# Kernel optimization log

Hardware: AMD Instinct MI355X
Metric: run time of the kernel (lower is better)

The kernel has to match this reference:

```python
import jax, jax.numpy as jnp
import numpy as np

N = 50000
DIM_IN = 256
HID = 64
OUT = 32
E1 = 800000
E2 = 1600000
BN_EPS = 1e-5


def _make_edges(rng, n, e):
    row = rng.integers(0, n, size=e).astype(np.int32)
    col = rng.integers(0, n, size=e).astype(np.int32)
    # gcn_norm without self loops: val = d^{-1/2}[row] * d^{-1/2}[col]
    deg = np.bincount(row, minlength=n) + 0.0
    deg_c = np.bincount(col, minlength=n) + 0.0
    dr = 1.0 / np.sqrt(np.maximum(deg, 1.0))
    dc = 1.0 / np.sqrt(np.maximum(deg_c, 1.0))
    val = (dr[row] * dc[col]).astype(np.float32)
    return row, col, val


def setup_inputs() -> dict:
    key = jax.random.key(0)
    ks = jax.random.split(key, 4)
    rng = np.random.default_rng(0)
    e1_row, e1_col, e1_val = _make_edges(rng, N, E1)
    e2_row, e2_col, e2_val = _make_edges(rng, N, E2)
    return {
        "x": jax.random.normal(ks[0], (N, DIM_IN), dtype=jnp.float32),
        "e1_row": jnp.asarray(e1_row), "e1_col": jnp.asarray(e1_col), "e1_val": jnp.asarray(e1_val),
        "e2_row": jnp.asarray(e2_row), "e2_col": jnp.asarray(e2_col), "e2_val": jnp.asarray(e2_val),
        "W_embed": jax.random.normal(ks[1], (DIM_IN, HID), dtype=jnp.float32) * (1.0 / np.sqrt(DIM_IN)),
        "b_embed": jnp.zeros((HID,), dtype=jnp.float32),
        "bn0_gamma": jnp.ones((2 * HID,), dtype=jnp.float32),
        "bn0_beta": jnp.zeros((2 * HID,), dtype=jnp.float32),
        "bn1_gamma": jnp.ones((4 * HID,), dtype=jnp.float32),
        "bn1_beta": jnp.zeros((4 * HID,), dtype=jnp.float32),
        "W_head": jax.random.normal(ks[2], (15 * HID, OUT), dtype=jnp.float32) * (1.0 / np.sqrt(15 * HID)),
        "b_head": jnp.zeros((OUT,), dtype=jnp.float32),
    }


def _spmm(row, col, val, x, n):
    # out[row] += val * x[col]  (sparse [n,n] @ dense [n,d])
    return jax.ops.segment_sum(val[:, None] * x[col], row, num_segments=n)


def _bn(v, gamma, beta):
    # BatchNorm1d training-mode math: per-feature mean / biased var over nodes
    m = jnp.mean(v, axis=0)
    var = jnp.mean(jnp.square(v - m), axis=0)
    return gamma * (v - m) * jax.lax.rsqrt(var + BN_EPS) + beta


def reference(x, e1_row, e1_col, e1_val, e2_row, e2_col, e2_val,
              W_embed, b_embed, bn0_gamma, bn0_beta, bn1_gamma, bn1_beta,
              W_head, b_head):
    n = x.shape[0]

    def conv(h):
        h1 = _spmm(e1_row, e1_col, e1_val, h, n)
        h2 = _spmm(e2_row, e2_col, e2_val, h, n)
        return jnp.concatenate([h1, h2], axis=1)

    h = jax.nn.relu(x @ W_embed + b_embed)          # [n, HID]
    xs = [h]
    c0 = _bn(conv(h), bn0_gamma, bn0_beta)           # [n, 2*HID]
    xs.append(c0)
    c1 = _bn(conv(c0), bn1_gamma, bn1_beta)          # [n, 4*HID]
    xs.append(c1)
    c2 = conv(c1)                                    # [n, 8*HID]
    xs.append(c2)
    j = jnp.concatenate(xs, axis=1)                  # [n, 15*HID]
    return j @ W_head + b_head                       # [n, OUT]
```

## Files before the change

kernel.cpp:

```cpp
#include <hip/hip_runtime.h>


#define NN  50000
#define E1N 800000
#define E2N 1600000
#define LD  960
#define NT  3125
#define NBKT 391
#define CHUNK 8192
#define G1B 98
#define G2B 196
#define NCG 7

typedef short bf16x8 __attribute__((ext_vector_type(8)));
typedef float f32x4  __attribute__((ext_vector_type(4)));
typedef float f32x2  __attribute__((ext_vector_type(2)));

__device__ __forceinline__ float bfl(unsigned int w) { return __uint_as_float(w << 16); }
__device__ __forceinline__ float bfh(unsigned int w) { return __uint_as_float(w & 0xFFFF0000u); }
__device__ __forceinline__ float bf2f(unsigned short u) { return __uint_as_float(((unsigned int)u) << 16); }
__device__ __forceinline__ unsigned short f2bf(float f) {
    unsigned int u = __float_as_uint(f);
    u += 0x7FFFu + ((u >> 16) & 1u);
    return (unsigned short)(u >> 16);
}
__device__ __forceinline__ unsigned int pack2(float a, float b) {
    return (unsigned int)f2bf(a) | ((unsigned int)f2bf(b) << 16);
}
__device__ __forceinline__ unsigned int packfp8(float a, float b, float c, float d) {
    int w = __builtin_amdgcn_cvt_pk_fp8_f32(a, b, 0, false);
    w     = __builtin_amdgcn_cvt_pk_fp8_f32(c, d, w, true);
    return (unsigned int)w;
}
__device__ __forceinline__ f32x2 pkfma(f32x2 a, f32x2 b, f32x2 c) {
#if __has_builtin(__builtin_elementwise_fma)
    return __builtin_elementwise_fma(a, b, c);
#else
    return (f32x2){fmaf(a[0], b[0], c[0]), fmaf(a[1], b[1], c[1])};
#endif
}
__device__ __forceinline__ f32x2 bf2(unsigned int w) {
    return (f32x2){bfl(w), bfh(w)};
}


__global__ __launch_bounds__(256) void zero_kernel(float* c, int nc) {
    int i = blockIdx.x * 256 + threadIdx.x;
    if (i < nc) c[i] = 0.f;
}

__global__ __launch_bounds__(256) void bucket_count_kernel(const int* __restrict__ r1,
                                                           const int* __restrict__ r2,
                                                           int* __restrict__ bc1, int* __restrict__ bc2) {
    __shared__ int cnt[NBKT];
    for (int t = threadIdx.x; t < NBKT; t += 256) cnt[t] = 0;
    __syncthreads();
    int blk = blockIdx.x;
    const int* r; int base, lim; int* bc;
    if (blk < G1B) { r = r1; base = blk * CHUNK; lim = min(base + CHUNK, E1N); bc = bc1 + blk * NBKT; }
    else { int b2 = blk - G1B; r = r2; base = b2 * CHUNK; lim = min(base + CHUNK, E2N); bc = bc2 + b2 * NBKT; }
    for (int i = base + threadIdx.x; i < lim; i += 256)
        atomicAdd(&cnt[r[i] >> 7], 1);
    __syncthreads();
    for (int t = threadIdx.x; t < NBKT; t += 256) bc[t] = cnt[t];
}

__global__ __launch_bounds__(512) void bucket_scan_kernel(int* __restrict__ bc1, int* __restrict__ bc2) {
    __shared__ int s[512];
    int t = threadIdx.x;
    int tot1 = 0, tot2 = 0;
    if (t < NBKT) {
        for (int b = 0; b < G1B; b++) tot1 += bc1[b * NBKT + t];
        for (int b = 0; b < G2B; b++) tot2 += bc2[b * NBKT + t];
    }
    s[t] = (t < NBKT) ? tot1 : 0;
    __syncthreads();
    for (int off = 1; off < 512; off <<= 1) {
        int v = (t >= off) ? s[t - off] : 0;
        __syncthreads(); s[t] += v; __syncthreads();
    }
    int base1 = ((t < NBKT) ? s[t] : 0) - tot1;
    __syncthreads();
    s[t] = (t < NBKT) ? tot2 : 0;
    __syncthreads();
    for (int off = 1; off < 512; off <<= 1) {
        int v = (t >= off) ? s[t - off] : 0;
        __syncthreads(); s[t] += v; __syncthreads();
    }
    int base2 = ((t < NBKT) ? s[t] : 0) - tot2;
    if (t < NBKT) {
        int run = base1;
        for (int b = 0; b < G1B; b++) { int v = bc1[b * NBKT + t]; bc1[b * NBKT + t] = run; run += v; }
        run = base2;
        for (int b = 0; b < G2B; b++) { int v = bc2[b * NBKT + t]; bc2[b * NBKT + t] = run; run += v; }
    }
}

__global__ __launch_bounds__(256) void bucket_place_kernel(
        const int* __restrict__ r1, const int* __restrict__ c1, const float* __restrict__ v1,
        const int* __restrict__ r2, const int* __restrict__ c2, const float* __restrict__ v2,
        const int* __restrict__ bc1, const int* __restrict__ bc2,
        uint2* __restrict__ T1, uint2* __restrict__ T2) {
    __shared__ int pos[NBKT];
    int blk = blockIdx.x;
    const int *r, *c; const float* v; int base, lim; const int* bc; uint2* T;
    if (blk < G1B) { r = r1; c = c1; v = v1; base = blk * CHUNK; lim = min(base + CHUNK, E1N);
                     bc = bc1 + blk * NBKT; T = T1; }
    else { int b2 = blk - G1B; r = r2; c = c2; v = v2; base = b2 * CHUNK; lim = min(base + CHUNK, E2N);
           bc = bc2 + b2 * NBKT; T = T2; }
    for (int t = threadIdx.x; t < NBKT; t += 256) pos[t] = bc[t];
    __syncthreads();
    for (int i = base + threadIdx.x; i < lim; i += 256) {
        int row = r[i];
        int p = atomicAdd(&pos[row >> 7], 1);
        T[p] = make_uint2(((unsigned)c[i] << 16) | (unsigned)row, __float_as_uint(v[i]));
    }
}

__global__ __launch_bounds__(256) void bucket_sort_kernel(
        const int* __restrict__ bb1, const uint2* __restrict__ T1, int* __restrict__ rp1, unsigned int* __restrict__ Ed1,
        const int* __restrict__ bb2, const uint2* __restrict__ T2, int* __restrict__ rp2, unsigned int* __restrict__ Ed2) {
    int b = blockIdx.x % NBKT;
    int g = blockIdx.x / NBKT;
    const int* bb = g ? bb2 : bb1;
    const uint2* T = g ? T2 : T1;
    int* rp = g ? rp2 : rp1;
    unsigned int* Ed = g ? Ed2 : Ed1;
    int EN = g ? E2N : E1N;
    int beg = bb[b];
    int end = (b == NBKT - 1) ? EN : bb[b + 1];
    int R0 = b * 128;
    int nrows = min(128, NN - R0);
    __shared__ int cnt[1024];
    __shared__ int cur[896];
    __shared__ int ps[256];
    int t = threadIdx.x;
    for (int i = t; i < 1024; i += 256) cnt[i] = 0;
    __syncthreads();
    for (int i = beg + t; i < end; i += 256) {
        unsigned int x = T[i].x;
        int lr = (x & 0xFFFFu) & 127;
        int cg = (int)(x >> 29);
        atomicAdd(&cnt[lr * NCG + cg + 1], 1);
    }
    __syncthreads();
    int b0 = t * 4;
    int c0 = cnt[b0], c1 = cnt[b0 + 1], c2 = cnt[b0 + 2], c3 = cnt[b0 + 3];
    int s1 = c0 + c1, s2 = s1 + c2, s3 = s2 + c3;
    ps[t] = s3;
    __syncthreads();
    for (int off = 1; off < 256; off <<= 1) {
        int v = (t >= off) ? ps[t - off] : 0;
        __syncthreads(); ps[t] += v; __syncthreads();
    }
    int base = (t > 0) ? ps[t - 1] : 0;
    cnt[b0] = base + c0; cnt[b0 + 1] = base + s1;
    cnt[b0 + 2] = base + s2; cnt[b0 + 3] = base + s3;
    __syncthreads();
    for (int k = t; k < 896; k += 256) cur[k] = beg + cnt[k];
    if (t < nrows) rp[R0 + t] = beg + cnt[t * NCG];
    if (b == NBKT - 1 && t == 0) rp[NN] = end;
    __syncthreads();
    for (int i = beg + t; i < end; i += 256) {
        uint2 rec = T[i];
        int lr = (rec.x & 0xFFFFu) & 127;
        int cg = (int)(rec.x >> 29);
        int p = atomicAdd(&cur[lr * NCG + cg], 1);
        Ed[p] = (rec.x & 0xFFFF0000u) | (unsigned)f2bf(__uint_as_float(rec.y));
    }
}

__global__ __launch_bounds__(256) void packw_kernel(const float* __restrict__ W, unsigned short* __restrict__ Wb,
                                                    int NC, int kbs, int total) {
    int i = blockIdx.x * 256 + threadIdx.x;
    if (i >= total) return;
    int lane  = i & 63;
    int kb    = (i >> 6) % kbs;
    int ctile = i / (kbs * 64);
    int n  = ctile * 16 + (lane & 15);
    int k0 = kb * 32 + (lane >> 4) * 8;
    unsigned short v[8];
    #pragma unroll
    for (int j = 0; j < 8; j++) v[j] = f2bf(W[(k0 + j) * NC + n]);
    *(uint4*)(Wb + (size_t)i * 8) = *(uint4*)v;
}

__global__ __launch_bounds__(256) void embed_mfma_kernel(const float* __restrict__ x,
                                                         const unsigned short* __restrict__ Wb,
                                                         const float* __restrict__ bias,
                                                         unsigned short* __restrict__ Jh) {
    int wave = threadIdx.x >> 6;
    int lane = threadIdx.x & 63;
    int tile = blockIdx.x * 4 + wave;
    if (tile >= NT) return;
    int m = lane & 15;
    int q = lane >> 4;
    const float* xr = x + (size_t)(tile * 16 + m) * 256 + q * 8;
    const unsigned short* bbase = Wb + (size_t)lane * 8;
    f32x4 acc[4];
    #pragma unroll
    for (int ct = 0; ct < 4; ct++) acc[ct] = (f32x4){0.f, 0.f, 0.f, 0.f};
    #pragma unroll
    for (int kb = 0; kb < 8; kb++) {
        float4 xa = *(const float4*)(xr + kb * 32);
        float4 xb = *(const float4*)(xr + kb * 32 + 4);
        unsigned short av[8];
        av[0] = f2bf(xa.x); av[1] = f2bf(xa.y); av[2] = f2bf(xa.z); av[3] = f2bf(xa.w);
        av[4] = f2bf(xb.x); av[5] = f2bf(xb.y); av[6] = f2bf(xb.z); av[7] = f2bf(xb.w);
        bf16x8 a = *(bf16x8*)av;
        #pragma unroll
        for (int ct = 0; ct < 4; ct++) {
            bf16x8 bfr = *(const bf16x8*)(bbase + (size_t)(ct * 8 + kb) * 512);
            acc[ct] = __builtin_amdgcn_mfma_f32_16x16x32_bf16(a, bfr, acc[ct], 0, 0, 0);
        }
    }
    #pragma unroll
    for (int ct = 0; ct < 4; ct++) {
        int col = ct * 16 + m;
        float bb = bias[col];
        #pragma unroll
        for (int r = 0; r < 4; r++) {
            float v = fmaxf(acc[ct][r] + bb, 0.f);
            Jh[(size_t)(tile * 16 + q * 4 + r) * LD + col] = f2bf(v);
        }
    }
}

template <int LPR>
__global__ __launch_bounds__(256) void spmm_bf16x8_kernel(
        const int* __restrict__ rp1, const unsigned int* __restrict__ ed1,
        const int* __restrict__ rp2, const unsigned int* __restrict__ ed2,
        const unsigned short* __restrict__ src, unsigned short* __restrict__ dst) {
    constexpr int ROWS = 64 / LPR;
    constexpr int SRCF = LPR * 8;
    constexpr int RPB  = ROWS * 4;
    constexpr int GB   = (NN + RPB - 1) / RPB;
    int g    = (blockIdx.x >= GB) ? 1 : 0;
    int bx   = blockIdx.x - g * GB;
    int wave = threadIdx.x >> 6;
    int lane = threadIdx.x & 63;
    int grp  = lane / LPR;
    int sub  = lane % LPR;
    int row  = (bx * 4 + wave) * ROWS + grp;
    const int*          rp = g ? rp2 : rp1;
    const unsigned int* ed = g ? ed2 : ed1;
    bool ok = row < NN;
    int beg = 0, end = 0;
    if (ok) { beg = rp[row]; end = rp[row + 1]; }

    f32x2 acc[4];
    #pragma unroll
    for (int u = 0; u < 4; u++) acc[u] = (f32x2){0.f, 0.f};
    const unsigned short* sbase = src + sub * 8;

    int j = beg;
    for (; j + 8 <= end; j += 8) {
        unsigned int e[8];
        #pragma unroll
        for (int u = 0; u < 8; u++) e[u] = ed[j + u];
        uint4 s[8];
        #pragma unroll
        for (int u = 0; u < 8; u++) s[u] = *(const uint4*)(sbase + (size_t)(e[u] >> 16) * LD);
        #pragma unroll
        for (int u = 0; u < 8; u++) {
            float v = bfl(e[u]);
            f32x2 vv = (f32x2){v, v};
            acc[0] = pkfma(vv, bf2(s[u].x), acc[0]);
            acc[1] = pkfma(vv, bf2(s[u].y), acc[1]);
            acc[2] = pkfma(vv, bf2(s[u].z), acc[2]);
            acc[3] = pkfma(vv, bf2(s[u].w), acc[3]);
        }
    }
    for (; j < end; j++) {
        unsigned int e = ed[j];
        float v = bfl(e);
        f32x2 vv = (f32x2){v, v};
        uint4 s = *(const uint4*)(sbase + (size_t)(e >> 16) * LD);
        acc[0] = pkfma(vv, bf2(s.x), acc[0]);
        acc[1] = pkfma(vv, bf2(s.y), acc[1]);
        acc[2] = pkfma(vv, bf2(s.z), acc[2]);
        acc[3] = pkfma(vv, bf2(s.w), acc[3]);
    }

    if (ok) {
        unsigned short* dp = dst + (size_t)row * LD + g * SRCF + sub * 8;
        uint4 o;
        o.x = pack2(acc[0][0], acc[0][1]); o.y = pack2(acc[1][0], acc[1][1]);
        o.z = pack2(acc[2][0], acc[2][1]); o.w = pack2(acc[3][0], acc[3][1]);
        *(uint4*)dp = o;
    }
}

template <int LPR>
__global__ __launch_bounds__(256) void spmm_fp8x16_kernel(
        const int* __restrict__ rp1, const unsigned int* __restrict__ ed1,
        const int* __restrict__ rp2, const unsigned int* __restrict__ ed2,
        const unsigned char* __restrict__ src8,
        unsigned short* __restrict__ dst) {
    constexpr int ROWS = 64 / LPR;
    constexpr int SRCF = LPR * 16;
    constexpr int RPB  = ROWS * 4;
    constexpr int GB   = (NN + RPB - 1) / RPB;
    int g    = (blockIdx.x >= GB) ? 1 : 0;
    int bx   = blockIdx.x - g * GB;
    int wave = threadIdx.x >> 6;
    int lane = threadIdx.x & 63;
    int grp  = lane / LPR;
    int sub  = lane % LPR;
    int row  = (bx * 4 + wave) * ROWS + grp;
    const int*          rp = g ? rp2 : rp1;
    const unsigned int* ed = g ? ed2 : ed1;
    bool ok = row < NN;
    int beg = 0, end = 0;
    if (ok) { beg = rp[row]; end = rp[row + 1]; }

    f32x2 acc[8];
    #pragma unroll
    for (int u = 0; u < 8; u++) acc[u] = (f32x2){0.f, 0.f};
    const unsigned char* sbase = src8 + sub * 16;

    int j = beg;
    for (; j + 8 <= end; j += 8) {
        unsigned int e[8];
        #pragma unroll
        for (int u = 0; u < 8; u++) e[u] = ed[j + u];
        uint4 s[8];
        #pragma unroll
        for (int u = 0; u < 8; u++) s[u] = *(const uint4*)(sbase + (size_t)(e[u] >> 16) * SRCF);
        #pragma unroll
        for (int u = 0; u < 8; u++) {
            float v = bfl(e[u]);
            f32x2 vv = (f32x2){v, v};
            acc[0] = pkfma(vv, __builtin_amdgcn_cvt_pk_f32_fp8(s[u].x, false), acc[0]);
            acc[1] = pkfma(vv, __builtin_amdgcn_cvt_pk_f32_fp8(s[u].x, true),  acc[1]);
            acc[2] = pkfma(vv, __builtin_amdgcn_cvt_pk_f32_fp8(s[u].y, false), acc[2]);
            acc[3] = pkfma(vv, __builtin_amdgcn_cvt_pk_f32_fp8(s[u].y, true),  acc[3]);
            acc[4] = pkfma(vv, __builtin_amdgcn_cvt_pk_f32_fp8(s[u].z, false), acc[4]);
            acc[5] = pkfma(vv, __builtin_amdgcn_cvt_pk_f32_fp8(s[u].z, true),  acc[5]);
            acc[6] = pkfma(vv, __builtin_amdgcn_cvt_pk_f32_fp8(s[u].w, false), acc[6]);
            acc[7] = pkfma(vv, __builtin_amdgcn_cvt_pk_f32_fp8(s[u].w, true),  acc[7]);
        }
    }
    for (; j < end; j++) {
        unsigned int e = ed[j];
        float v = bfl(e);
        f32x2 vv = (f32x2){v, v};
        uint4 s = *(const uint4*)(sbase + (size_t)(e >> 16) * SRCF);
        acc[0] = pkfma(vv, __builtin_amdgcn_cvt_pk_f32_fp8(s.x, false), acc[0]);
        acc[1] = pkfma(vv, __builtin_amdgcn_cvt_pk_f32_fp8(s.x, true),  acc[1]);
        acc[2] = pkfma(vv, __builtin_amdgcn_cvt_pk_f32_fp8(s.y, false), acc[2]);
        acc[3] = pkfma(vv, __builtin_amdgcn_cvt_pk_f32_fp8(s.y, true),  acc[3]);
        acc[4] = pkfma(vv, __builtin_amdgcn_cvt_pk_f32_fp8(s.z, false), acc[4]);
        acc[5] = pkfma(vv, __builtin_amdgcn_cvt_pk_f32_fp8(s.z, true),  acc[5]);
        acc[6] = pkfma(vv, __builtin_amdgcn_cvt_pk_f32_fp8(s.w, false), acc[6]);
        acc[7] = pkfma(vv, __builtin_amdgcn_cvt_pk_f32_fp8(s.w, true),  acc[7]);
    }

    if (ok) {
        unsigned short* dp = dst + (size_t)row * LD + g * SRCF + sub * 16;
        uint4 o1, o2;
        o1.x = pack2(acc[0][0], acc[0][1]); o1.y = pack2(acc[1][0], acc[1][1]);
        o1.z = pack2(acc[2][0], acc[2][1]); o1.w = pack2(acc[3][0], acc[3][1]);
        o2.x = pack2(acc[4][0], acc[4][1]); o2.y = pack2(acc[5][0], acc[5][1]);
        o2.z = pack2(acc[6][0], acc[6][1]); o2.w = pack2(acc[7][0], acc[7][1]);
        *(uint4*)dp = o1;
        *(uint4*)(dp + 8) = o2;
    }
}

template <int F>
__global__ __launch_bounds__(256) void bn_stats_kernel(const unsigned short* __restrict__ c,
                                                       float* sum, float* sumsq) {
    constexpr int SL = 256 / F;
    int f  = threadIdx.x % F;
    int sl = threadIdx.x / F;
    float s = 0.f, ss = 0.f;
    for (int r = blockIdx.x * SL + sl; r < NN; r += gridDim.x * SL) {
        float v = bf2f(c[(size_t)r * LD + f]);
        s += v; ss += v * v;
    }
    __shared__ float ls[256], lss[256];
    ls[threadIdx.x] = s; lss[threadIdx.x] = ss;
    __syncthreads();
    if (sl == 0) {
        #pragma unroll
        for (int u = 1; u < SL; u++) { s += ls[f + u * F]; ss += lss[f + u * F]; }
        atomicAdd(&sum[f], s);
        atomicAdd(&sumsq[f], ss);
    }
}

__global__ void bn_finalize_kernel(const float* sum, const float* sumsq, const float* __restrict__ gamma,
                                   const float* __restrict__ beta, float* scale, float* shift, int F) {
    int f = blockIdx.x * blockDim.x + threadIdx.x;
    if (f >= F) return;
    float m   = sum[f] * (1.0f / NN);
    float var = sumsq[f] * (1.0f / NN) - m * m;
    float sc  = gamma[f] * rsqrtf(var + 1e-5f);
    scale[f] = sc;
    shift[f] = beta[f] - m * sc;
}

template <int F>
__global__ __launch_bounds__(256) void bn_apply_kernel(unsigned short* __restrict__ c,
                                                       const float* __restrict__ scale,
                                                       const float* __restrict__ shift) {
    constexpr int FV = F / 4;
    int idx  = blockIdx.x * 256 + threadIdx.x;
    int node = idx / FV;
    int fo   = (idx % FV) * 4;
    if (node >= NN) return;
    unsigned short* p = c + (size_t)node * LD + fo;
    uint2 v = *(uint2*)p;
    float a0 = bfl(v.x), a1 = bfh(v.x), a2 = bfl(v.y), a3 = bfh(v.y);
    float4 sc = *(const float4*)(scale + fo);
    float4 sh = *(const float4*)(shift + fo);
    a0 = fmaf(a0, sc.x, sh.x);
    a1 = fmaf(a1, sc.y, sh.y);
    a2 = fmaf(a2, sc.z, sh.z);
    a3 = fmaf(a3, sc.w, sh.w);
    v.x = pack2(a0, a1); v.y = pack2(a2, a3);
    *(uint2*)p = v;
}

__global__ __launch_bounds__(256) void bn_apply_fp8_kernel(unsigned short* __restrict__ c,
                                                           unsigned char* __restrict__ c8,
                                                           const float* __restrict__ scale,
                                                           const float* __restrict__ shift) {
    int idx  = blockIdx.x * 256 + threadIdx.x;
    int node = idx >> 6;
    int fo   = (idx & 63) * 4;
    if (node >= NN) return;
    unsigned short* p = c + (size_t)node * LD + fo;
    uint2 v = *(uint2*)p;
    float a0 = bfl(v.x), a1 = bfh(v.x), a2 = bfl(v.y), a3 = bfh(v.y);
    float4 sc = *(const float4*)(scale + fo);
    float4 sh = *(const float4*)(shift + fo);
    a0 = fmaf(a0, sc.x, sh.x);
    a1 = fmaf(a1, sc.y, sh.y);
    a2 = fmaf(a2, sc.z, sh.z);
    a3 = fmaf(a3, sc.w, sh.w);
    v.x = pack2(a0, a1); v.y = pack2(a2, a3);
    *(uint2*)p = v;
    *(unsigned int*)(c8 + (size_t)node * 256 + fo) = packfp8(a0, a1, a2, a3);
}

__global__ __launch_bounds__(256) void head_mfma_kernel(const unsigned short* __restrict__ Jh,
                                                        const unsigned short* __restrict__ Wb,
                                                        const float* __restrict__ b,
                                                        float* __restrict__ out) {
    int wave = threadIdx.x >> 6;
    int lane = threadIdx.x & 63;
    int tile = blockIdx.x * 4 + wave;
    if (tile >= NT) return;
    int m = lane & 15;
    int q = lane >> 4;
    const unsigned short* arow  = Jh + (size_t)(tile * 16 + m) * LD + q * 8;
    const unsigned short* bbase = Wb + (size_t)lane * 8;
    f32x4 acc0 = {0.f, 0.f, 0.f, 0.f};
    f32x4 acc1 = {0.f, 0.f, 0.f, 0.f};
    #pragma unroll 5
    for (int kb = 0; kb < 30; kb++) {
        bf16x8 a  = *(const bf16x8*)(arow + kb * 32);
        bf16x8 b0 = *(const bf16x8*)(bbase + (size_t)kb * 512);
        bf16x8 b1 = *(const bf16x8*)(bbase + (size_t)(30 + kb) * 512);
        acc0 = __builtin_amdgcn_mfma_f32_16x16x32_bf16(a, b0, acc0, 0, 0, 0);
        acc1 = __builtin_amdgcn_mfma_f32_16x16x32_bf16(a, b1, acc1, 0, 0, 0);
    }
    int col = m;
    float b0 = b[col], b1 = b[16 + col];
    #pragma unroll
    for (int r = 0; r < 4; r++) {
        float* op = out + (size_t)(tile * 16 + q * 4 + r) * 32 + col;
        op[0]  = acc0[r] + b0;
        op[16] = acc1[r] + b1;
    }
}


extern "C" void kernel_launch(void* const* d_in, const int* in_sizes, int n_in,
                              void* d_out, int out_size, void* d_ws, size_t ws_size,
                              hipStream_t stream) {
    const float* x      = (const float*)d_in[0];
    const int*   e1_row = (const int*)d_in[1];
    const int*   e1_col = (const int*)d_in[2];
    const float* e1_val = (const float*)d_in[3];
    const int*   e2_row = (const int*)d_in[4];
    const int*   e2_col = (const int*)d_in[5];
    const float* e2_val = (const float*)d_in[6];
    const float* W_emb  = (const float*)d_in[7];
    const float* b_emb  = (const float*)d_in[8];
    const float* bn0_g  = (const float*)d_in[9];
    const float* bn0_b  = (const float*)d_in[10];
    const float* bn1_g  = (const float*)d_in[11];
    const float* bn1_b  = (const float*)d_in[12];
    const float* W_head = (const float*)d_in[13];
    const float* b_head = (const float*)d_in[14];
    float* out = (float*)d_out;

    char* ws = (char*)d_ws;
    auto alloc = [&](size_t bytes) -> char* {
        char* p = ws;
        ws += (bytes + 255) & ~(size_t)255;
        return p;
    };
    int*   rp1   = (int*)alloc((NN + 1) * 4);
    int*   rp2   = (int*)alloc((NN + 1) * 4);
    int*   bc1   = (int*)alloc((size_t)G1B * NBKT * 4);
    int*   bc2   = (int*)alloc((size_t)G2B * NBKT * 4);
    unsigned int* Ed1 = (unsigned int*)alloc((size_t)E1N * 4);
    unsigned int* Ed2 = (unsigned int*)alloc((size_t)E2N * 4);
    float* stats = (float*)alloc(1536 * 4);
    unsigned short* Wbh  = (unsigned short*)alloc(3840 * 8 * 2);
    unsigned short* Wbe  = (unsigned short*)alloc(2048 * 8 * 2);
    unsigned char*  C1f8 = (unsigned char*)alloc((size_t)NN * 256);
    unsigned short* Jh   = (unsigned short*)alloc((size_t)NN * LD * 2);
    uint2* T1 = (uint2*)Jh;
    uint2* T2 = T1 + E1N;

    float* sum0   = stats;        float* sq0    = stats + 128;
    float* sum1   = stats + 256;  float* sq1    = stats + 512;
    float* scale0 = stats + 768;  float* shift0 = stats + 896;
    float* scale1 = stats + 1024; float* shift1 = stats + 1280;

    zero_kernel<<<3, 256, 0, stream>>>(stats, 768);
    bucket_count_kernel<<<G1B + G2B, 256, 0, stream>>>(e1_row, e2_row, bc1, bc2);
    bucket_scan_kernel<<<1, 512, 0, stream>>>(bc1, bc2);
    bucket_place_kernel<<<G1B + G2B, 256, 0, stream>>>(e1_row, e1_col, e1_val,
                                                       e2_row, e2_col, e2_val, bc1, bc2, T1, T2);
    bucket_sort_kernel<<<2 * NBKT, 256, 0, stream>>>(bc1, T1, rp1, Ed1, bc2, T2, rp2, Ed2);
    packw_kernel<<<15, 256, 0, stream>>>(W_head, Wbh, 32, 30, 3840);
    packw_kernel<<<8, 256, 0, stream>>>(W_emb, Wbe, 64, 8, 2048);

    embed_mfma_kernel<<<(NT + 3) / 4, 256, 0, stream>>>(x, Wbe, b_emb, Jh);

    spmm_bf16x8_kernel<8><<<2 * ((NN + 31) / 32), 256, 0, stream>>>(rp1, Ed1, rp2, Ed2, Jh, Jh + 64);
    bn_stats_kernel<128><<<512, 256, 0, stream>>>(Jh + 64, sum0, sq0);
    bn_finalize_kernel<<<1, 128, 0, stream>>>(sum0, sq0, bn0_g, bn0_b, scale0, shift0, 128);
    bn_apply_kernel<128><<<(NN * 32 + 255) / 256, 256, 0, stream>>>(Jh + 64, scale0, shift0);

    spmm_bf16x8_kernel<16><<<2 * (NN / 16), 256, 0, stream>>>(rp1, Ed1, rp2, Ed2, Jh + 64, Jh + 192);
    bn_stats_kernel<256><<<512, 256, 0, stream>>>(Jh + 192, sum1, sq1);
    bn_finalize_kernel<<<1, 256, 0, stream>>>(sum1, sq1, bn1_g, bn1_b, scale1, shift1, 256);
    bn_apply_fp8_kernel<<<(NN * 64 + 255) / 256, 256, 0, stream>>>(Jh + 192, C1f8, scale1, shift1);

    spmm_fp8x16_kernel<16><<<2 * (NN / 16), 256, 0, stream>>>(rp1, Ed1, rp2, Ed2, C1f8, Jh + 448);

    head_mfma_kernel<<<(NT + 3) / 4, 256, 0, stream>>>(Jh, Wbh, b_head, out);
}
```

Before: 533.9 us.

## Split SpMM feature columns into slices launched as separate passes

```diff
diff --git a/kernel.cpp b/kernel.cpp
--- a/kernel.cpp
+++ b/kernel.cpp
@@ -11,6 +11,7 @@
 #define G1B 98
 #define G2B 196
 #define NCG 7
+#define GBS 782
 
 typedef short bf16x8 __attribute__((ext_vector_type(8)));
 typedef float f32x4  __attribute__((ext_vector_type(4)));
@@ -226,22 +227,19 @@
     }
 }
 
-template <int LPR>
-__global__ __launch_bounds__(256) void spmm_bf16x8_kernel(
+template <int NSL>
+__global__ __launch_bounds__(256) void spmm_bf16_slice_kernel(
         const int* __restrict__ rp1, const unsigned int* __restrict__ ed1,
         const int* __restrict__ rp2, const unsigned int* __restrict__ ed2,
-        const unsigned short* __restrict__ src, unsigned short* __restrict__ dst) {
-    constexpr int ROWS = 64 / LPR;
-    constexpr int SRCF = LPR * 8;
-    constexpr int RPB  = ROWS * 4;
-    constexpr int GB   = (NN + RPB - 1) / RPB;
-    int g    = (blockIdx.x >= GB) ? 1 : 0;
-    int bx   = blockIdx.x - g * GB;
+        const unsigned short* __restrict__ src, unsigned short* __restrict__ dst,
+        int slice) {
+    int g    = (blockIdx.x >= GBS) ? 1 : 0;
+    int bx   = blockIdx.x - g * GBS;
     int wave = threadIdx.x >> 6;
     int lane = threadIdx.x & 63;
-    int grp  = lane / LPR;
-    int sub  = lane % LPR;
-    int row  = (bx * 4 + wave) * ROWS + grp;
+    int grp  = lane >> 2;
+    int sub  = lane & 3;
+    int row  = (bx * 4 + wave) * 16 + grp;
     const int*          rp = g ? rp2 : rp1;
     const unsigned int* ed = g ? ed2 : ed1;
     bool ok = row < NN;
@@ -251,7 +249,7 @@
     f32x2 acc[4];
     #pragma unroll
     for (int u = 0; u < 4; u++) acc[u] = (f32x2){0.f, 0.f};
-    const unsigned short* sbase = src + sub * 8;
+    const unsigned short* sbase = src + slice * 32 + sub * 8;
 
     int j = beg;
     for (; j + 8 <= end; j += 8) {
@@ -283,7 +281,7 @@
     }
 
     if (ok) {
-        unsigned short* dp = dst + (size_t)row * LD + g * SRCF + sub * 8;
+        unsigned short* dp = dst + (size_t)row * LD + g * (NSL * 32) + slice * 32 + sub * 8;
         uint4 o;
         o.x = pack2(acc[0][0], acc[0][1]); o.y = pack2(acc[1][0], acc[1][1]);
         o.z = pack2(acc[2][0], acc[2][1]); o.w = pack2(acc[3][0], acc[3][1]);
@@ -291,23 +289,18 @@
     }
 }
 
-template <int LPR>
-__global__ __launch_bounds__(256) void spmm_fp8x16_kernel(
+__global__ __launch_bounds__(256) void spmm_fp8_slice_kernel(
         const int* __restrict__ rp1, const unsigned int* __restrict__ ed1,
         const int* __restrict__ rp2, const unsigned int* __restrict__ ed2,
         const unsigned char* __restrict__ src8,
-        unsigned short* __restrict__ dst) {
-    constexpr int ROWS = 64 / LPR;
-    constexpr int SRCF = LPR * 16;
-    constexpr int RPB  = ROWS * 4;
-    constexpr int GB   = (NN + RPB - 1) / RPB;
-    int g    = (blockIdx.x >= GB) ? 1 : 0;
-    int bx   = blockIdx.x - g * GB;
+        unsigned short* __restrict__ dst, int slice) {
+    int g    = (blockIdx.x >= GBS) ? 1 : 0;
+    int bx   = blockIdx.x - g * GBS;
     int wave = threadIdx.x >> 6;
     int lane = threadIdx.x & 63;
-    int grp  = lane / LPR;
-    int sub  = lane % LPR;
-    int row  = (bx * 4 + wave) * ROWS + grp;
+    int grp  = lane >> 2;
+    int sub  = lane & 3;
+    int row  = (bx * 4 + wave) * 16 + grp;
     const int*          rp = g ? rp2 : rp1;
     const unsigned int* ed = g ? ed2 : ed1;
     bool ok = row < NN;
@@ -317,7 +310,7 @@
     f32x2 acc[8];
     #pragma unroll
     for (int u = 0; u < 8; u++) acc[u] = (f32x2){0.f, 0.f};
-    const unsigned char* sbase = src8 + sub * 16;
+    const unsigned char* sbase = src8 + slice * 64 + sub * 16;
 
     int j = beg;
     for (; j + 8 <= end; j += 8) {
@@ -326,7 +319,7 @@
         for (int u = 0; u < 8; u++) e[u] = ed[j + u];
         uint4 s[8];
         #pragma unroll
-        for (int u = 0; u < 8; u++) s[u] = *(const uint4*)(sbase + (size_t)(e[u] >> 16) * SRCF);
+        for (int u = 0; u < 8; u++) s[u] = *(const uint4*)(sbase + (size_t)(e[u] >> 16) * 256);
         #pragma unroll
         for (int u = 0; u < 8; u++) {
             float v = bfl(e[u]);
@@ -345,7 +338,7 @@
         unsigned int e = ed[j];
         float v = bfl(e);
         f32x2 vv = (f32x2){v, v};
-        uint4 s = *(const uint4*)(sbase + (size_t)(e >> 16) * SRCF);
+        uint4 s = *(const uint4*)(sbase + (size_t)(e >> 16) * 256);
         acc[0] = pkfma(vv, __builtin_amdgcn_cvt_pk_f32_fp8(s.x, false), acc[0]);
         acc[1] = pkfma(vv, __builtin_amdgcn_cvt_pk_f32_fp8(s.x, true),  acc[1]);
         acc[2] = pkfma(vv, __builtin_amdgcn_cvt_pk_f32_fp8(s.y, false), acc[2]);
@@ -357,7 +350,7 @@
     }
 
     if (ok) {
-        unsigned short* dp = dst + (size_t)row * LD + g * SRCF + sub * 16;
+        unsigned short* dp = dst + (size_t)row * LD + g * 256 + slice * 64 + sub * 16;
         uint4 o1, o2;
         o1.x = pack2(acc[0][0], acc[0][1]); o1.y = pack2(acc[1][0], acc[1][1]);
         o1.z = pack2(acc[2][0], acc[2][1]); o1.w = pack2(acc[3][0], acc[3][1]);
@@ -534,17 +527,20 @@
 
     embed_mfma_kernel<<<(NT + 3) / 4, 256, 0, stream>>>(x, Wbe, b_emb, Jh);
 
-    spmm_bf16x8_kernel<8><<<2 * ((NN + 31) / 32), 256, 0, stream>>>(rp1, Ed1, rp2, Ed2, Jh, Jh + 64);
+    for (int s = 0; s < 2; s++)
+        spmm_bf16_slice_kernel<2><<<2 * GBS, 256, 0, stream>>>(rp1, Ed1, rp2, Ed2, Jh, Jh + 64, s);
     bn_stats_kernel<128><<<512, 256, 0, stream>>>(Jh + 64, sum0, sq0);
     bn_finalize_kernel<<<1, 128, 0, stream>>>(sum0, sq0, bn0_g, bn0_b, scale0, shift0, 128);
     bn_apply_kernel<128><<<(NN * 32 + 255) / 256, 256, 0, stream>>>(Jh + 64, scale0, shift0);
 
-    spmm_bf16x8_kernel<16><<<2 * (NN / 16), 256, 0, stream>>>(rp1, Ed1, rp2, Ed2, Jh + 64, Jh + 192);
+    for (int s = 0; s < 4; s++)
+        spmm_bf16_slice_kernel<4><<<2 * GBS, 256, 0, stream>>>(rp1, Ed1, rp2, Ed2, Jh + 64, Jh + 192, s);
     bn_stats_kernel<256><<<512, 256, 0, stream>>>(Jh + 192, sum1, sq1);
     bn_finalize_kernel<<<1, 256, 0, stream>>>(sum1, sq1, bn1_g, bn1_b, scale1, shift1, 256);
     bn_apply_fp8_kernel<<<(NN * 64 + 255) / 256, 256, 0, stream>>>(Jh + 192, C1f8, scale1, shift1);
 
-    spmm_fp8x16_kernel<16><<<2 * (NN / 16), 256, 0, stream>>>(rp1, Ed1, rp2, Ed2, C1f8, Jh + 448);
+    for (int s = 0; s < 4; s++)
+        spmm_fp8_slice_kernel<<<2 * GBS, 256, 0, stream>>>(rp1, Ed1, rp2, Ed2, C1f8, Jh + 448, s);
 
     head_mfma_kernel<<<(NT + 3) / 4, 256, 0, stream>>>(Jh, Wbh, b_head, out);
 }
```

New measurement: 641.4 us. 20.1% more time.
